# Kernel tuning notes

Measured on AMD Instinct MI355X. Metric: run time of the kernel, lower is better.

Reference implementation:

```python
import jax, jax.numpy as jnp
import numpy as np

N_NODES = 100000
K = 50000  # ceil(ratio * N) with ratio = nodes_out / nodes_in = 0.5


def setup_inputs() -> dict:
    key = jax.random.key(0)
    k1, k2, k3 = jax.random.split(key, 3)
    x = jax.random.normal(k1, (N_NODES, 256), dtype=jnp.float32)
    edge_index = jax.random.randint(k2, (2, 3200000), 0, N_NODES, dtype=jnp.int64)
    weight = jax.random.normal(k3, (256,), dtype=jnp.float32)
    return {"x": x, "edge_index": edge_index, "weight": weight}


def reference(x, edge_index, weight):
    # --- PyG TopKPooling forward ---
    # score_i = tanh( <x_i, w> / ||w|| )
    score = jnp.tanh((x @ weight) / jnp.linalg.norm(weight))  # [N]
    # select top-k nodes by score
    top_scores, perm = jax.lax.top_k(score, K)  # [K], [K]
    # gather features and gate by score (multiplier)
    x_out = x[perm] * top_scores[:, None]  # [K, C]
    # --- filter_adj: keep edges whose endpoints both survive, remap ids ---
    mapping = jnp.full((x.shape[0],), -1, dtype=edge_index.dtype)
    mapping = mapping.at[perm].set(jnp.arange(K, dtype=edge_index.dtype))
    new_edges = mapping[edge_index]  # [2, E], -1 where endpoint dropped
    valid = (new_edges[0] >= 0) & (new_edges[1] >= 0)
    # fixed-shape output: invalid edges marked -1 (torch returns a compacted
    # variable-length tensor; we keep E fixed for jit-compatibility)
    edge_out = jnp.where(valid[None, :], new_edges, -1)
    return x_out, edge_out
```

## Files before the change

### kernel.cpp

```cpp
#include <hip/hip_runtime.h>
#include <math.h>

#define N_NODES 100000
#define N_FEAT  256
#define K_SEL   50000
#define N_EDGES 3200000
#define NBUCKET 65536

#define GATHER_BLOCKS (K_SEL / 4)
#define EDGE_BLOCKS   (N_EDGES / (4 * 256))

__device__ __forceinline__ unsigned long long descKey(double z) {
    unsigned long long u = (unsigned long long)__double_as_longlong(z);
    unsigned long long a = (u >> 63) ? ~u : (u | 0x8000000000000000ULL);
    return ~a;
}

__device__ __forceinline__ unsigned int bucketOfFloat(float zf) {
    unsigned int u = __float_as_uint(zf);
    unsigned int a = (u >> 31) ? ~u : (u | 0x80000000u);
    return (~a) >> 16;
}

__global__ void init_kernel(const float* __restrict__ w, double* __restrict__ norm,
                            int* __restrict__ hist) {
    __shared__ double sd[256];
    int t = blockIdx.x * blockDim.x + threadIdx.x;
    hist[t] = 0;
    if (blockIdx.x == 0) {
        int tt = threadIdx.x;
        double v = (double)w[tt];
        sd[tt] = v * v;
        __syncthreads();
        for (int off = 128; off > 0; off >>= 1) {
            if (tt < off) sd[tt] += sd[tt + off];
            __syncthreads();
        }
        if (tt == 0) norm[0] = sqrt(sd[0]);
    }
}

__global__ void score_kernel(const float* __restrict__ x, const float* __restrict__ w,
                             unsigned long long* __restrict__ key64,
                             float* __restrict__ dotf, int* __restrict__ hist) {
    int row  = (int)((blockIdx.x * blockDim.x + threadIdx.x) >> 6);
    int lane = threadIdx.x & 63;
    if (row >= N_NODES) return;
    const float4 xv = ((const float4*)(x + (size_t)row * N_FEAT))[lane];
    const float4 wv = ((const float4*)w)[lane];
    double acc = (double)xv.x * (double)wv.x + (double)xv.y * (double)wv.y +
                 (double)xv.z * (double)wv.z + (double)xv.w * (double)wv.w;
    for (int m = 32; m >= 1; m >>= 1) acc += __shfl_xor(acc, m, 64);
    if (lane == 0) {
        key64[row] = descKey(acc);
        float df = (float)acc;
        dotf[row] = df;
        atomicAdd(&hist[bucketOfFloat(df)], 1);
    }
}

__global__ void __launch_bounds__(1024) scan_kernel(const int4* __restrict__ hist4,
                                                    int* __restrict__ start) {
    __shared__ int sums[1024];
    int t = threadIdx.x;
    int4 v[16];
#pragma unroll
    for (int j = 0; j < 16; ++j) v[j] = hist4[t * 16 + j];
    int s = 0;
#pragma unroll
    for (int j = 0; j < 16; ++j) { s += v[j].x + v[j].y + v[j].z + v[j].w; }
    sums[t] = s;
    __syncthreads();
    for (int off = 1; off < 1024; off <<= 1) {
        int vv = (t >= off) ? sums[t - off] : 0;
        __syncthreads();
        sums[t] += vv;
        __syncthreads();
    }
    int run = (t == 0) ? 0 : sums[t - 1];
    int4* start4 = (int4*)start;
#pragma unroll
    for (int j = 0; j < 16; ++j) {
        int4 o;
        o.x = run; run += v[j].x;
        o.y = run; run += v[j].y;
        o.z = run; run += v[j].z;
        o.w = run; run += v[j].w;
        start4[t * 16 + j] = o;
    }
}

__global__ void scatter_kernel(const unsigned long long* __restrict__ key64,
                               const float* __restrict__ dotf,
                               int* __restrict__ start,
                               unsigned long long* __restrict__ slotKey,
                               int* __restrict__ slotIdx) {
    int i = blockIdx.x * blockDim.x + threadIdx.x;
    if (i >= N_NODES) return;
    int b = (int)bucketOfFloat(dotf[i]);
    int pos = atomicAdd(&start[b], 1);
    slotKey[pos] = key64[i];
    slotIdx[pos] = i;
}

__global__ void rank_kernel(const unsigned long long* __restrict__ slotKey,
                            const int* __restrict__ slotIdx,
                            const int* __restrict__ start, const int* __restrict__ hist,
                            const float* __restrict__ dotf,
                            int* __restrict__ mapping, int* __restrict__ perm,
                            float* __restrict__ selDot) {
    int s = blockIdx.x * blockDim.x + threadIdx.x;
    if (s >= N_NODES) return;
    unsigned long long myKey = slotKey[s];
    int i = slotIdx[s];
    float df = dotf[i];
    int b = (int)bucketOfFloat(df);
    int end = start[b];
    int cnt = hist[b];
    int st = end - cnt;
    int rank = 0;
    for (int t = st; t < end; ++t) {
        unsigned long long k = slotKey[t];
        if (k < myKey || (k == myKey && slotIdx[t] < i)) ++rank;
    }
    int p = st + rank;
    if (p < K_SEL) {
        mapping[i] = p;
        perm[p] = i;
        selDot[p] = df;
    } else {
        mapping[i] = -1;
    }
}

__global__ void out_kernel(const float* __restrict__ x, const int* __restrict__ perm,
                           const float* __restrict__ selDot,
                           const double* __restrict__ normp,
                           const int* __restrict__ ei, const int* __restrict__ mapping,
                           float* __restrict__ out) {
    if (blockIdx.x < GATHER_BLOCKS) {
        int tid = blockIdx.x * 256 + threadIdx.x;
        int r = tid >> 6;
        int c = (tid & 63) << 2;
        int src = perm[r];
        float sc = tanhf(selDot[r] / (float)normp[0]);
        float4 v = *(const float4*)(x + (size_t)src * N_FEAT + c);
        float4 o;
        o.x = v.x * sc; o.y = v.y * sc; o.z = v.z * sc; o.w = v.w * sc;
        *(float4*)(out + (size_t)r * N_FEAT + c) = o;
    } else {
        int tid = (blockIdx.x - GATHER_BLOCKS) * 256 + threadIdx.x;
        int e = tid << 2;
        int4 a = *(const int4*)(ei + e);
        int4 b = *(const int4*)(ei + N_EDGES + e);
        float* oeu = out + (size_t)K_SEL * N_FEAT;
        float* oev = oeu + N_EDGES;
        int m0 = mapping[a.x], m1 = mapping[a.y], m2 = mapping[a.z], m3 = mapping[a.w];
        int n0 = mapping[b.x], n1 = mapping[b.y], n2 = mapping[b.z], n3 = mapping[b.w];
        float4 ou, ov;
        bool v0 = (m0 >= 0) && (n0 >= 0);
        bool v1 = (m1 >= 0) && (n1 >= 0);
        bool v2 = (m2 >= 0) && (n2 >= 0);
        bool v3 = (m3 >= 0) && (n3 >= 0);
        ou.x = v0 ? (float)m0 : -1.0f; ov.x = v0 ? (float)n0 : -1.0f;
        ou.y = v1 ? (float)m1 : -1.0f; ov.y = v1 ? (float)n1 : -1.0f;
        ou.z = v2 ? (float)m2 : -1.0f; ov.z = v2 ? (float)n2 : -1.0f;
        ou.w = v3 ? (float)m3 : -1.0f; ov.w = v3 ? (float)n3 : -1.0f;
        *(float4*)(oeu + e) = ou;
        *(float4*)(oev + e) = ov;
    }
}

extern "C" void kernel_launch(void* const* d_in, const int* in_sizes, int n_in,
                              void* d_out, int out_size, void* d_ws, size_t ws_size,
                              hipStream_t stream) {
    const float* x  = (const float*)d_in[0];
    const int*   ei = (const int*)d_in[1];
    const float* w  = (const float*)d_in[2];
    float* out = (float*)d_out;

    char* p = (char*)d_ws;
    double* d_norm = (double*)p;                          p += 16;
    unsigned long long* key64   = (unsigned long long*)p; p += (size_t)N_NODES * 8;
    unsigned long long* slotKey = (unsigned long long*)p; p += (size_t)N_NODES * 8;
    float* dotf   = (float*)p;  p += (size_t)N_NODES * 4;
    int*   mapping= (int*)p;    p += (size_t)N_NODES * 4;
    int*   slotIdx= (int*)p;    p += (size_t)N_NODES * 4;
    int*   perm   = (int*)p;    p += (size_t)K_SEL * 4;
    float* selDot = (float*)p;  p += (size_t)K_SEL * 4;
    int*   hist   = (int*)p;    p += (size_t)NBUCKET * 4;
    int*   start  = (int*)p;    p += (size_t)NBUCKET * 4;

    init_kernel<<<NBUCKET / 256, 256, 0, stream>>>(w, d_norm, hist);

    int waves_blocks = (N_NODES * 64 + 255) / 256;
    score_kernel<<<waves_blocks, 256, 0, stream>>>(x, w, key64, dotf, hist);

    scan_kernel<<<1, 1024, 0, stream>>>((const int4*)hist, start);

    int node_blocks = (N_NODES + 255) / 256;
    scatter_kernel<<<node_blocks, 256, 0, stream>>>(key64, dotf, start, slotKey, slotIdx);

    rank_kernel<<<node_blocks, 256, 0, stream>>>(slotKey, slotIdx, start, hist, dotf,
                                                 mapping, perm, selDot);

    out_kernel<<<GATHER_BLOCKS + EDGE_BLOCKS, 256, 0, stream>>>(x, perm, selDot, d_norm,
                                                                ei, mapping, out);
}
```

Measured before the change: 319.8 us.

## Parallelize bucket scan across blocks, skip rank work, use nontemporal IO

Replaces the single-block 1024-thread histogram scan with a 256-block chunked scan. A last-block-done counter computes the chunk offsets, which scatter and rank then add back. The rank kernel exits early for buckets that start past K and skips the comparison loop for singleton buckets. The output kernel switches to nontemporal loads and stores for the edge stream and gathered rows. These add an atomic counter and threadfence protocol that could be fragile.

```diff
diff --git a/kernel.cpp b/kernel.cpp
--- a/kernel.cpp
+++ b/kernel.cpp
@@ -6,9 +6,13 @@
 #define K_SEL   50000
 #define N_EDGES 3200000
 #define NBUCKET 65536
+#define NCHUNK  256
 
 #define GATHER_BLOCKS (K_SEL / 4)
 #define EDGE_BLOCKS   (N_EDGES / (4 * 256))
+
+typedef float __attribute__((ext_vector_type(4))) floatx4;
+typedef int   __attribute__((ext_vector_type(4))) intx4;
 
 __device__ __forceinline__ unsigned long long descKey(double z) {
     unsigned long long u = (unsigned long long)__double_as_longlong(z);
@@ -23,10 +27,11 @@
 }
 
 __global__ void init_kernel(const float* __restrict__ w, double* __restrict__ norm,
-                            int* __restrict__ hist) {
+                            int* __restrict__ hist, int* __restrict__ counter) {
     __shared__ double sd[256];
     int t = blockIdx.x * blockDim.x + threadIdx.x;
     hist[t] = 0;
+    if (t == 0) counter[0] = 0;
     if (blockIdx.x == 0) {
         int tt = threadIdx.x;
         double v = (double)w[tt];
@@ -59,46 +64,55 @@
     }
 }
 
-__global__ void __launch_bounds__(1024) scan_kernel(const int4* __restrict__ hist4,
-                                                    int* __restrict__ start) {
-    __shared__ int sums[1024];
-    int t = threadIdx.x;
-    int4 v[16];
-#pragma unroll
-    for (int j = 0; j < 16; ++j) v[j] = hist4[t * 16 + j];
-    int s = 0;
-#pragma unroll
-    for (int j = 0; j < 16; ++j) { s += v[j].x + v[j].y + v[j].z + v[j].w; }
-    sums[t] = s;
-    __syncthreads();
-    for (int off = 1; off < 1024; off <<= 1) {
-        int vv = (t >= off) ? sums[t - off] : 0;
-        __syncthreads();
-        sums[t] += vv;
-        __syncthreads();
-    }
-    int run = (t == 0) ? 0 : sums[t - 1];
-    int4* start4 = (int4*)start;
-#pragma unroll
-    for (int j = 0; j < 16; ++j) {
-        int4 o;
-        o.x = run; run += v[j].x;
-        o.y = run; run += v[j].y;
-        o.z = run; run += v[j].z;
-        o.w = run; run += v[j].w;
-        start4[t * 16 + j] = o;
-    }
+__global__ void __launch_bounds__(256) scan_kernel(const int* __restrict__ hist,
+                                                   int* __restrict__ start,
+                                                   int* __restrict__ chunkSums,
+                                                   int* __restrict__ chunkOff,
+                                                   int* __restrict__ counter) {
+    __shared__ int s[256];
+    __shared__ int lastFlag;
+    int c = blockIdx.x, t = threadIdx.x;
+    int v = hist[c * 256 + t];
+    s[t] = v;
+    __syncthreads();
+    for (int off = 1; off < 256; off <<= 1) {
+        int add = (t >= off) ? s[t - off] : 0;
+        __syncthreads();
+        s[t] += add;
+        __syncthreads();
+    }
+    start[c * 256 + t] = s[t] - v;
+    if (t == 0) {
+        atomicExch(&chunkSums[c], s[255]);
+        __threadfence();
+        int old = atomicAdd(counter, 1);
+        lastFlag = (old == NCHUNK - 1);
+    }
+    __syncthreads();
+    if (!lastFlag) return;
+    int w = atomicAdd(&chunkSums[t], 0);
+    __syncthreads();
+    s[t] = w;
+    __syncthreads();
+    for (int off = 1; off < 256; off <<= 1) {
+        int add = (t >= off) ? s[t - off] : 0;
+        __syncthreads();
+        s[t] += add;
+        __syncthreads();
+    }
+    chunkOff[t] = s[t] - w;
 }
 
 __global__ void scatter_kernel(const unsigned long long* __restrict__ key64,
                                const float* __restrict__ dotf,
                                int* __restrict__ start,
+                               const int* __restrict__ chunkOff,
                                unsigned long long* __restrict__ slotKey,
                                int* __restrict__ slotIdx) {
     int i = blockIdx.x * blockDim.x + threadIdx.x;
     if (i >= N_NODES) return;
     int b = (int)bucketOfFloat(dotf[i]);
-    int pos = atomicAdd(&start[b], 1);
+    int pos = atomicAdd(&start[b], 1) + chunkOff[b >> 8];
     slotKey[pos] = key64[i];
     slotIdx[pos] = i;
 }
@@ -106,22 +120,29 @@
 __global__ void rank_kernel(const unsigned long long* __restrict__ slotKey,
                             const int* __restrict__ slotIdx,
                             const int* __restrict__ start, const int* __restrict__ hist,
+                            const int* __restrict__ chunkOff,
                             const float* __restrict__ dotf,
                             int* __restrict__ mapping, int* __restrict__ perm,
                             float* __restrict__ selDot) {
     int s = blockIdx.x * blockDim.x + threadIdx.x;
     if (s >= N_NODES) return;
-    unsigned long long myKey = slotKey[s];
     int i = slotIdx[s];
     float df = dotf[i];
     int b = (int)bucketOfFloat(df);
-    int end = start[b];
+    int end = start[b] + chunkOff[b >> 8];
     int cnt = hist[b];
     int st = end - cnt;
+    if (st >= K_SEL) {
+        mapping[i] = -1;
+        return;
+    }
     int rank = 0;
-    for (int t = st; t < end; ++t) {
-        unsigned long long k = slotKey[t];
-        if (k < myKey || (k == myKey && slotIdx[t] < i)) ++rank;
+    if (cnt > 1) {
+        unsigned long long myKey = slotKey[s];
+        for (int t = st; t < end; ++t) {
+            unsigned long long k = slotKey[t];
+            if (k < myKey || (k == myKey && slotIdx[t] < i)) ++rank;
+        }
     }
     int p = st + rank;
     if (p < K_SEL) {
@@ -145,19 +166,19 @@
         int src = perm[r];
         float sc = tanhf(selDot[r] / (float)normp[0]);
         float4 v = *(const float4*)(x + (size_t)src * N_FEAT + c);
-        float4 o;
+        floatx4 o;
         o.x = v.x * sc; o.y = v.y * sc; o.z = v.z * sc; o.w = v.w * sc;
-        *(float4*)(out + (size_t)r * N_FEAT + c) = o;
+        __builtin_nontemporal_store(o, (floatx4*)(out + (size_t)r * N_FEAT + c));
     } else {
         int tid = (blockIdx.x - GATHER_BLOCKS) * 256 + threadIdx.x;
         int e = tid << 2;
-        int4 a = *(const int4*)(ei + e);
-        int4 b = *(const int4*)(ei + N_EDGES + e);
+        intx4 a = __builtin_nontemporal_load((const intx4*)(ei + e));
+        intx4 b = __builtin_nontemporal_load((const intx4*)(ei + N_EDGES + e));
         float* oeu = out + (size_t)K_SEL * N_FEAT;
         float* oev = oeu + N_EDGES;
         int m0 = mapping[a.x], m1 = mapping[a.y], m2 = mapping[a.z], m3 = mapping[a.w];
         int n0 = mapping[b.x], n1 = mapping[b.y], n2 = mapping[b.z], n3 = mapping[b.w];
-        float4 ou, ov;
+        floatx4 ou, ov;
         bool v0 = (m0 >= 0) && (n0 >= 0);
         bool v1 = (m1 >= 0) && (n1 >= 0);
         bool v2 = (m2 >= 0) && (n2 >= 0);
@@ -166,8 +187,8 @@
         ou.y = v1 ? (float)m1 : -1.0f; ov.y = v1 ? (float)n1 : -1.0f;
         ou.z = v2 ? (float)m2 : -1.0f; ov.z = v2 ? (float)n2 : -1.0f;
         ou.w = v3 ? (float)m3 : -1.0f; ov.w = v3 ? (float)n3 : -1.0f;
-        *(float4*)(oeu + e) = ou;
-        *(float4*)(oev + e) = ov;
+        __builtin_nontemporal_store(ou, (floatx4*)(oeu + e));
+        __builtin_nontemporal_store(ov, (floatx4*)(oev + e));
     }
 }
 
@@ -183,26 +204,30 @@
     double* d_norm = (double*)p;                          p += 16;
     unsigned long long* key64   = (unsigned long long*)p; p += (size_t)N_NODES * 8;
     unsigned long long* slotKey = (unsigned long long*)p; p += (size_t)N_NODES * 8;
-    float* dotf   = (float*)p;  p += (size_t)N_NODES * 4;
-    int*   mapping= (int*)p;    p += (size_t)N_NODES * 4;
-    int*   slotIdx= (int*)p;    p += (size_t)N_NODES * 4;
-    int*   perm   = (int*)p;    p += (size_t)K_SEL * 4;
-    float* selDot = (float*)p;  p += (size_t)K_SEL * 4;
-    int*   hist   = (int*)p;    p += (size_t)NBUCKET * 4;
-    int*   start  = (int*)p;    p += (size_t)NBUCKET * 4;
-
-    init_kernel<<<NBUCKET / 256, 256, 0, stream>>>(w, d_norm, hist);
+    float* dotf    = (float*)p; p += (size_t)N_NODES * 4;
+    int*   mapping = (int*)p;   p += (size_t)N_NODES * 4;
+    int*   slotIdx = (int*)p;   p += (size_t)N_NODES * 4;
+    int*   perm    = (int*)p;   p += (size_t)K_SEL * 4;
+    float* selDot  = (float*)p; p += (size_t)K_SEL * 4;
+    int*   hist    = (int*)p;   p += (size_t)NBUCKET * 4;
+    int*   start   = (int*)p;   p += (size_t)NBUCKET * 4;
+    int*   chunkSums = (int*)p; p += (size_t)NCHUNK * 4;
+    int*   chunkOff  = (int*)p; p += (size_t)NCHUNK * 4;
+    int*   counter   = (int*)p; p += 16;
+
+    init_kernel<<<NBUCKET / 256, 256, 0, stream>>>(w, d_norm, hist, counter);
 
     int waves_blocks = (N_NODES * 64 + 255) / 256;
     score_kernel<<<waves_blocks, 256, 0, stream>>>(x, w, key64, dotf, hist);
 
-    scan_kernel<<<1, 1024, 0, stream>>>((const int4*)hist, start);
+    scan_kernel<<<NCHUNK, 256, 0, stream>>>(hist, start, chunkSums, chunkOff, counter);
 
     int node_blocks = (N_NODES + 255) / 256;
-    scatter_kernel<<<node_blocks, 256, 0, stream>>>(key64, dotf, start, slotKey, slotIdx);
-
-    rank_kernel<<<node_blocks, 256, 0, stream>>>(slotKey, slotIdx, start, hist, dotf,
-                                                 mapping, perm, selDot);
+    scatter_kernel<<<node_blocks, 256, 0, stream>>>(key64, dotf, start, chunkOff,
+                                                    slotKey, slotIdx);
+
+    rank_kernel<<<node_blocks, 256, 0, stream>>>(slotKey, slotIdx, start, hist,
+                                                 chunkOff, dotf, mapping, perm, selDot);
 
     out_kernel<<<GATHER_BLOCKS + EDGE_BLOCKS, 256, 0, stream>>>(x, perm, selDot, d_norm,
                                                                 ei, mapping, out);
```

After: 307.3 us, median of 2. 3.9% less time.
